# Kernel optimization log

Measured on AMD Instinct MI355X. Metric: run time of the kernel, lower is better.

Reference implementation:

```python
import jax, jax.numpy as jnp
import numpy as np

K = 3
PAD = (K - 1) // 2


def _conv1d(x, w, b):
    # x: [B, T, C]; w: [F, C, K] (torch OIH layout); conv over T, 'same' padding
    y = jax.lax.conv_general_dilated(x.transpose(0, 2, 1), w, (1,), [(PAD, PAD)],
                                     dimension_numbers=('NCH', 'OIH', 'NCH'))
    return (y + b[None, :, None]).transpose(0, 2, 1)


def _ln(x, g, b, eps=1e-5):
    m = x.mean(-1, keepdims=True)
    v = ((x - m) ** 2).mean(-1, keepdims=True)
    return (x - m) * jax.lax.rsqrt(v + eps) * g + b


def _predictor(x, p):
    # Conv1d -> ReLU -> LN -> Conv1d -> ReLU -> LN -> Linear(F,1) -> ReLU -> squeeze
    w1, b1, g1, be1, w2, b2, g2, be2, wl, bl = p
    h = _ln(jax.nn.relu(_conv1d(x, w1, b1)), g1, be1)
    h = _ln(jax.nn.relu(_conv1d(h, w2, b2)), g2, be2)
    return jax.nn.relu(jnp.einsum('btf,f->bt', h, wl) + bl)  # [B, T]


def _length_regulate(x, dur, max_len):
    # Gather-based frame expansion: frame t comes from token i = searchsorted(cumsum(dur), t, 'right')
    cs = jnp.cumsum(dur, axis=1)                       # [B, T]
    t = jnp.arange(max_len)                            # [M]
    idx = jax.vmap(lambda c: jnp.searchsorted(c, t, side='right'))(cs)  # [B, M]
    valid = t[None, :] < cs[:, -1:]                    # [B, M]
    idx = jnp.minimum(idx, x.shape[1] - 1)
    out = jnp.take_along_axis(x, idx[:, :, None], axis=1)  # [B, M, C]
    out = jnp.where(valid[:, :, None], out, jnp.zeros((), x.dtype))
    mel_len = jnp.minimum(cs[:, -1], max_len)
    return out, mel_len


def _bucketize(x, boundaries):
    # torch.bucketize(right=False): first boundary > x  ==  searchsorted(side='right')
    return jnp.searchsorted(boundaries, x, side='right')


def setup_inputs() -> dict:
    key = jax.random.key(0)
    ks = jax.random.split(key, 12)
    B, T, M, C, F, NB = 32, 256, 2048, 256, 256, 256
    inp = {}
    inp['inputs'] = jax.random.normal(ks[0], (B, T, C), jnp.float32)
    inp['true_duration'] = jax.random.randint(ks[1], (B, T), 0, 16)
    inp['true_pitch'] = jax.random.uniform(ks[2], (B, M), jnp.float32) * 300.0
    inp['true_energy'] = jax.random.uniform(ks[3], (B, M), jnp.float32) * 200.0
    inp['mel_max_len'] = M
    inp['pitch_q'] = jnp.linspace(0.0, 300.0, NB - 1)
    inp['energy_q'] = jnp.linspace(0.0, 200.0, NB - 1)

    def pred_params(k, cin):
        kk = jax.random.split(k, 3)
        return [0.02 * jax.random.normal(kk[0], (F, cin, K)), jnp.zeros((F,)),
                jnp.ones((F,)), jnp.zeros((F,)),
                0.02 * jax.random.normal(kk[1], (F, F, K)), jnp.zeros((F,)),
                jnp.ones((F,)), jnp.zeros((F,)),
                0.02 * jax.random.normal(kk[2], (F,)), jnp.zeros(())]

    names = ['w1', 'b1', 'g1', 'be1', 'w2', 'b2', 'g2', 'be2', 'wl', 'bl']
    for i, pre in enumerate(['dp', 'pp', 'ep']):
        for n, v in zip(names, pred_params(ks[4 + i], C)):
            inp[pre + '_' + n] = v
    inp['pitch_emb'] = 0.02 * jax.random.normal(ks[8], (NB, C))
    inp['energy_emb'] = 0.02 * jax.random.normal(ks[9], (NB, C))
    return inp


def reference(inputs, true_duration, true_pitch, true_energy, mel_max_len,
              pitch_q, energy_q,
              dp_w1, dp_b1, dp_g1, dp_be1, dp_w2, dp_b2, dp_g2, dp_be2, dp_wl, dp_bl,
              pp_w1, pp_b1, pp_g1, pp_be1, pp_w2, pp_b2, pp_g2, pp_be2, pp_wl, pp_bl,
              ep_w1, ep_b1, ep_g1, ep_be1, ep_w2, ep_b2, ep_g2, ep_be2, ep_wl, ep_bl,
              pitch_emb, energy_emb):
    # Training path: expansion uses true_duration, embeddings use true pitch/energy.
    dp = (dp_w1, dp_b1, dp_g1, dp_be1, dp_w2, dp_b2, dp_g2, dp_be2, dp_wl, dp_bl)
    pp = (pp_w1, pp_b1, pp_g1, pp_be1, pp_w2, pp_b2, pp_g2, pp_be2, pp_wl, pp_bl)
    ep = (ep_w1, ep_b1, ep_g1, ep_be1, ep_w2, ep_b2, ep_g2, ep_be2, ep_wl, ep_bl)
    durations = _predictor(inputs, dp)                       # [B, T], alpha=1.0
    outputs, mel_len = _length_regulate(inputs, true_duration, mel_max_len)  # [B, M, C]
    pitches = _predictor(outputs, pp)                        # [B, M]
    outputs = outputs + pitch_emb[_bucketize(true_pitch, pitch_q)]
    energies = _predictor(outputs, ep)                       # [B, M]
    outputs = outputs + energy_emb[_bucketize(true_energy, energy_q)]
    return outputs, durations, pitches, energies, mel_len
```

## Files before the change

kernel.cpp:

```cpp
#include <hip/hip_runtime.h>
#include <hip/hip_bf16.h>
#include <stdint.h>

#define DUR_OFF 16777216
#define PIT_OFF 16785408
#define ENE_OFF 16850944
#define MEL_OFF 16916480

typedef __attribute__((ext_vector_type(8))) short short8;
typedef __attribute__((ext_vector_type(4))) float f32x4;

__device__ __forceinline__ void async16(const void* g, void* l) {
  __builtin_amdgcn_global_load_lds((__attribute__((address_space(1))) void*)g,
                                   (__attribute__((address_space(3))) void*)l, 16, 0, 0);
}

__device__ __forceinline__ unsigned short bfu(float f) {
  __hip_bfloat16 h = __float2bfloat16(f);
  return __builtin_bit_cast(unsigned short, h);
}
__device__ __forceinline__ float f_from_bf(unsigned short u) {
  return __builtin_bit_cast(float, (unsigned)u << 16);
}

__global__ void zero2_kernel(__hip_bfloat16* __restrict__ xb, __hip_bfloat16* __restrict__ h1,
                             __hip_bfloat16* __restrict__ M1, __hip_bfloat16* __restrict__ M2) {
  int buf = blockIdx.x >> 6, sub = blockIdx.x & 63;
  int b = sub >> 1, top = sub & 1;
  __hip_bfloat16* p; int L;
  if (buf == 0) { p = xb; L = 256; }
  else if (buf == 1) { p = h1; L = 256; }
  else if (buf == 2) { p = M1; L = 2048; }
  else { p = M2; L = 2048; }
  size_t row = (size_t)b * (L + 2) + (top ? (L + 1) : 0);
  p[row * 256 + threadIdx.x] = __float2bfloat16(0.0f);
}

__global__ void packfrag_kernel(const float* __restrict__ w0, const float* __restrict__ w1,
                                const float* __restrict__ w2, const float* __restrict__ w3,
                                const float* __restrict__ w4, const float* __restrict__ w5,
                                __hip_bfloat16* __restrict__ wpbase) {
  int t = blockIdx.x * 256 + threadIdx.x;
  int wsel = t / 24576;
  int rem = t % 24576;
  const float* w = wsel == 0 ? w0 : wsel == 1 ? w1 : wsel == 2 ? w2
                 : wsel == 3 ? w3 : wsel == 4 ? w4 : w5;
  __hip_bfloat16* wp = wpbase + (size_t)wsel * 196608;
  int L = rem & 63;
  int ks = (rem >> 6) & 7;
  int q = rem >> 9;
  int tap = q % 3, r = q / 3;
  int ni = r & 3, fb = r >> 2;
  int f = fb * 64 + ni * 16 + (L & 15);
  int cb = ks * 32 + ((L >> 4) << 3);
  short8 o;
#pragma unroll
  for (int e = 0; e < 8; ++e)
    o[e] = (short)bfu(w[((size_t)f * 256 + cb + e) * 3 + tap]);
  *(short8*)(wp + (size_t)rem * 8) = o;
}

__global__ void cvt_pad_kernel(const float* __restrict__ x, __hip_bfloat16* __restrict__ xb) {
  int idx = blockIdx.x * 256 + threadIdx.x;
  float4 v = ((const float4*)x)[idx];
  int c4 = idx & 63;
  int rowi = idx >> 6;
  int b = rowi >> 8, t = rowi & 255;
  ushort4 o;
  o.x = bfu(v.x); o.y = bfu(v.y); o.z = bfu(v.z); o.w = bfu(v.w);
  ((ushort4*)(xb + ((size_t)b * 258 + t + 1) * 256))[c4] = o;
}

__global__ void gather_kernel(const float* __restrict__ x, const int* __restrict__ dur,
                              __hip_bfloat16* __restrict__ outB, float* __restrict__ mel) {
  __shared__ int scs[256];
  __shared__ int sidx[64];
  __shared__ int sval[64];
  int bch = blockIdx.x >> 5;
  int m0 = (blockIdx.x & 31) << 6;
  int tid = threadIdx.x;
  scs[tid] = dur[bch * 256 + tid];
  __syncthreads();
  for (int off = 1; off < 256; off <<= 1) {
    int add = (tid >= off) ? scs[tid - off] : 0;
    __syncthreads();
    scs[tid] += add;
    __syncthreads();
  }
  int total = scs[255];
  if (tid == 0 && (blockIdx.x & 31) == 0)
    mel[bch] = (float)(total < 2048 ? total : 2048);
  if (tid < 64) {
    int m = m0 + tid;
    int lo = 0, hi = 256;
    while (lo < hi) { int mid = (lo + hi) >> 1; if (scs[mid] <= m) lo = mid + 1; else hi = mid; }
    sidx[tid] = lo < 255 ? lo : 255;
    sval[tid] = (m < total);
  }
  __syncthreads();
  int lane = tid & 63, rs = tid >> 6;
  for (int r = rs; r < 64; r += 4) {
    float4 v = make_float4(0.f, 0.f, 0.f, 0.f);
    if (sval[r]) v = ((const float4*)(x + ((size_t)bch * 256 + sidx[r]) * 256))[lane];
    ushort4 o;
    o.x = bfu(v.x); o.y = bfu(v.y); o.z = bfu(v.z); o.w = bfu(v.w);
    ((ushort4*)(outB + ((size_t)bch * 2050 + m0 + r + 1) * 256))[lane] = o;
  }
}

__global__ void addemb_kernel(const float* __restrict__ tp, const float* __restrict__ te,
                              const float* __restrict__ pq, const float* __restrict__ eq,
                              const float* __restrict__ pemb, const float* __restrict__ eemb,
                              const __hip_bfloat16* __restrict__ M1, __hip_bfloat16* __restrict__ M2,
                              float* __restrict__ out) {
  __shared__ float sp[255], se[255];
  __shared__ int sip[64], sie[64];
  int bch = blockIdx.x >> 5;
  int m0 = (blockIdx.x & 31) << 6;
  int tid = threadIdx.x;
  if (tid < 255) { sp[tid] = pq[tid]; se[tid] = eq[tid]; }
  __syncthreads();
  if (tid < 64) {
    float xv = tp[bch * 2048 + m0 + tid];
    int lo = 0, hi = 255;
    while (lo < hi) { int mid = (lo + hi) >> 1; if (sp[mid] <= xv) lo = mid + 1; else hi = mid; }
    sip[tid] = lo;
    float ev = te[bch * 2048 + m0 + tid];
    lo = 0; hi = 255;
    while (lo < hi) { int mid = (lo + hi) >> 1; if (se[mid] <= ev) lo = mid + 1; else hi = mid; }
    sie[tid] = lo;
  }
  __syncthreads();
  int lane = tid & 63, rs = tid >> 6;
  for (int r = rs; r < 64; r += 4) {
    ushort4 mv = ((const ushort4*)(M1 + ((size_t)bch * 2050 + m0 + r + 1) * 256))[lane];
    float4 ep = ((const float4*)(pemb + (size_t)sip[r] * 256))[lane];
    float4 ee = ((const float4*)(eemb + (size_t)sie[r] * 256))[lane];
    float4 v;
    v.x = f_from_bf(mv.x) + ep.x; v.y = f_from_bf(mv.y) + ep.y;
    v.z = f_from_bf(mv.z) + ep.z; v.w = f_from_bf(mv.w) + ep.w;
    ushort4 o;
    o.x = bfu(v.x); o.y = bfu(v.y); o.z = bfu(v.z); o.w = bfu(v.w);
    ((ushort4*)(M2 + ((size_t)bch * 2050 + m0 + r + 1) * 256))[lane] = o;
    float4 w;
    w.x = v.x + ee.x; w.y = v.y + ee.y; w.z = v.z + ee.z; w.w = v.w + ee.w;
    ((float4*)(out + ((size_t)bch * 2048 + m0 + r) * 256))[lane] = w;
  }
}

__device__ __forceinline__ void loadB4(const char* Wb, int s, short8* dst) {
  int tap = s >> 3, ks = s & 7;
#pragma unroll
  for (int ni = 0; ni < 4; ++ni)
    dst[ni] = *(const short8*)(Wb + ((((ni * 3 + tap) << 3) + ks) << 10));
}

template <int EPI, int TM>
__global__ __launch_bounds__(256, 2)
void pred_gemm(const __hip_bfloat16* __restrict__ Ap, const __hip_bfloat16* __restrict__ Wf,
               const float* __restrict__ bias, const float* __restrict__ gamma,
               const float* __restrict__ beta, const float* __restrict__ wl,
               const float* __restrict__ blp, __hip_bfloat16* __restrict__ Hout,
               float* __restrict__ Sout, int L) {
  constexpr int MI = TM / 16;
  constexpr int ABYTES = (TM + 2) * 512;
  __shared__ char lA[ABYTES];
  __shared__ float lred[TM * 8];
  __shared__ float lstat[TM * 2];

  const int tid = threadIdx.x;
  const int wid = tid >> 6;
  const int lane = tid & 63;
  const int wn = wid;
  const int tiles = L / TM;
  const int b = blockIdx.x / tiles;
  const int t0 = (blockIdx.x % tiles) * TM;

  const char* Asrc = (const char*)(Ap + ((size_t)b * (L + 2) + t0) * 256);
#pragma unroll
  for (int j = 0; j < (ABYTES + 4095) / 4096; ++j) {
    int off = j * 4096 + tid * 16;
    if (off < ABYTES) {
      int so = off ^ (((off >> 9) & 7) << 4);
      async16(Asrc + so, lA + off);
    }
  }

  const char* Wb = (const char*)Wf + (size_t)wn * 98304 + lane * 16;

  f32x4 acc[MI][4];
  const f32x4 zero4 = {0.f, 0.f, 0.f, 0.f};
#pragma unroll
  for (int i = 0; i < MI; ++i)
#pragma unroll
    for (int j = 0; j < 4; ++j) acc[i][j] = zero4;

  short8 bA[4], bB[4];
  loadB4(Wb, 0, bA);

  __syncthreads();

  const int rlane = lane & 15;
  const int colp = (lane >> 4) << 4;
#pragma unroll
  for (int s = 0; s < 24; ++s) {
    const int tap = s >> 3, ks = s & 7;
    short8* cur = (s & 1) ? bB : bA;
    short8* nxt = (s & 1) ? bA : bB;
    if (s < 23) loadB4(Wb, s + 1, nxt);
    const int xorv = ((tap + rlane) & 7) << 4;
    short8 av[MI];
#pragma unroll
    for (int mi = 0; mi < MI; ++mi) {
      int a = (tap + (mi << 4) + rlane) * 512 + (ks << 6) + colp;
      av[mi] = *(const short8*)(lA + (a ^ xorv));
    }
#pragma unroll
    for (int mi = 0; mi < MI; ++mi)
#pragma unroll
      for (int ni = 0; ni < 4; ++ni)
        acc[mi][ni] =
            __builtin_amdgcn_mfma_f32_16x16x32_bf16(av[mi], cur[ni], acc[mi][ni], 0, 0, 0);
  }

  const int cb0 = (wn << 6) + rlane;
  float bi[4], gg[4], bb[4];
#pragma unroll
  for (int ni = 0; ni < 4; ++ni) {
    int col = cb0 + (ni << 4);
    bi[ni] = bias[col]; gg[ni] = gamma[col]; bb[ni] = beta[col];
  }
  const int rbase = (lane >> 4) << 2;
#pragma unroll
  for (int mi = 0; mi < MI; ++mi) {
#pragma unroll
    for (int j = 0; j < 4; ++j) {
      float s = 0.f, s2 = 0.f;
#pragma unroll
      for (int ni = 0; ni < 4; ++ni) {
        float r = fmaxf(acc[mi][ni][j] + bi[ni], 0.f);
        s += r; s2 += r * r;
      }
#pragma unroll
      for (int d = 1; d < 16; d <<= 1) { s += __shfl_xor(s, d); s2 += __shfl_xor(s2, d); }
      if ((lane & 15) == 0) {
        int row = (mi << 4) + rbase + j;
        lred[row * 8 + wn] = s;
        lred[row * 8 + 4 + wn] = s2;
      }
    }
  }
  __syncthreads();
  if (tid < TM) {
    float s = lred[tid * 8] + lred[tid * 8 + 1] + lred[tid * 8 + 2] + lred[tid * 8 + 3];
    float s2 = lred[tid * 8 + 4] + lred[tid * 8 + 5] + lred[tid * 8 + 6] + lred[tid * 8 + 7];
    float mean = s * (1.f / 256.f);
    float var = fmaxf(s2 * (1.f / 256.f) - mean * mean, 0.f);
    lstat[tid * 2] = mean;
    lstat[tid * 2 + 1] = rsqrtf(var + 1e-5f);
  }
  __syncthreads();

  if constexpr (EPI == 0) {
#pragma unroll
    for (int mi = 0; mi < MI; ++mi) {
#pragma unroll
      for (int j = 0; j < 4; ++j) {
        int row = (mi << 4) + rbase + j;
        float mean = lstat[row * 2], rstd = lstat[row * 2 + 1];
        __hip_bfloat16* hp = Hout + ((size_t)b * (L + 2) + t0 + row + 1) * 256 + cb0;
#pragma unroll
        for (int ni = 0; ni < 4; ++ni) {
          float r = fmaxf(acc[mi][ni][j] + bi[ni], 0.f);
          hp[ni << 4] = __float2bfloat16((r - mean) * rstd * gg[ni] + bb[ni]);
        }
      }
    }
  } else {
    float wlv[4];
#pragma unroll
    for (int ni = 0; ni < 4; ++ni) wlv[ni] = wl[cb0 + (ni << 4)];
#pragma unroll
    for (int mi = 0; mi < MI; ++mi) {
#pragma unroll
      for (int j = 0; j < 4; ++j) {
        int row = (mi << 4) + rbase + j;
        float mean = lstat[row * 2], rstd = lstat[row * 2 + 1];
        float ds = 0.f;
#pragma unroll
        for (int ni = 0; ni < 4; ++ni) {
          float r = fmaxf(acc[mi][ni][j] + bi[ni], 0.f);
          ds += ((r - mean) * rstd * gg[ni] + bb[ni]) * wlv[ni];
        }
#pragma unroll
        for (int d = 1; d < 16; d <<= 1) ds += __shfl_xor(ds, d);
        if ((lane & 15) == 0) lred[row * 8 + wn] = ds;
      }
    }
    __syncthreads();
    if (tid < TM) {
      float z = lred[tid * 8] + lred[tid * 8 + 1] + lred[tid * 8 + 2] + lred[tid * 8 + 3] + blp[0];
      Sout[(size_t)b * L + t0 + tid] = fmaxf(z, 0.f);
    }
  }
}

extern "C" void kernel_launch(void* const* d_in, const int* in_sizes, int n_in,
                              void* d_out, int out_size, void* d_ws, size_t ws_size,
                              hipStream_t stream) {
  const float* x = (const float*)d_in[0];
  const int* dur = (const int*)d_in[1];
  const float* tp = (const float*)d_in[2];
  const float* te = (const float*)d_in[3];
  const float* pq = (const float*)d_in[5];
  const float* eq = (const float*)d_in[6];
  const float* pemb = (const float*)d_in[37];
  const float* eemb = (const float*)d_in[38];

  char* ws = (char*)d_ws;
  __hip_bfloat16* wpb = (__hip_bfloat16*)ws;
  __hip_bfloat16* wp[6];
  for (int i = 0; i < 6; ++i) wp[i] = wpb + (size_t)i * 196608;
  __hip_bfloat16* xb = (__hip_bfloat16*)(ws + 2359296);
  __hip_bfloat16* h1dp = (__hip_bfloat16*)(ws + 6586368);
  __hip_bfloat16* M1 = (__hip_bfloat16*)(ws + 10813440);
  __hip_bfloat16* M2 = (__hip_bfloat16*)(ws + 44400640);

  float* out = (float*)d_out;

  zero2_kernel<<<256, 256, 0, stream>>>(xb, h1dp, M1, M2);
  packfrag_kernel<<<576, 256, 0, stream>>>((const float*)d_in[7], (const float*)d_in[11],
                                           (const float*)d_in[17], (const float*)d_in[21],
                                           (const float*)d_in[27], (const float*)d_in[31], wpb);
  cvt_pad_kernel<<<2048, 256, 0, stream>>>(x, xb);

  pred_gemm<0, 64><<<128, 256, 0, stream>>>(xb, wp[0], (const float*)d_in[8],
                                            (const float*)d_in[9], (const float*)d_in[10],
                                            nullptr, nullptr, h1dp, nullptr, 256);
  pred_gemm<1, 64><<<128, 256, 0, stream>>>(h1dp, wp[1], (const float*)d_in[12],
                                            (const float*)d_in[13], (const float*)d_in[14],
                                            (const float*)d_in[15], (const float*)d_in[16],
                                            nullptr, out + DUR_OFF, 256);

  gather_kernel<<<1024, 256, 0, stream>>>(x, dur, M1, out + MEL_OFF);

  pred_gemm<0, 128><<<512, 256, 0, stream>>>(M1, wp[2], (const float*)d_in[18],
                                             (const float*)d_in[19], (const float*)d_in[20],
                                             nullptr, nullptr, M2, nullptr, 2048);
  pred_gemm<1, 128><<<512, 256, 0, stream>>>(M2, wp[3], (const float*)d_in[22],
                                             (const float*)d_in[23], (const float*)d_in[24],
                                             (const float*)d_in[25], (const float*)d_in[26],
                                             nullptr, out + PIT_OFF, 2048);

  addemb_kernel<<<1024, 256, 0, stream>>>(tp, te, pq, eq, pemb, eemb, M1, M2, out);

  pred_gemm<0, 128><<<512, 256, 0, stream>>>(M2, wp[4], (const float*)d_in[28],
                                             (const float*)d_in[29], (const float*)d_in[30],
                                             nullptr, nullptr, M1, nullptr, 2048);
  pred_gemm<1, 128><<<512, 256, 0, stream>>>(M1, wp[5], (const float*)d_in[32],
                                             (const float*)d_in[33], (const float*)d_in[34],
                                             (const float*)d_in[35], (const float*)d_in[36],
                                             nullptr, out + ENE_OFF, 2048);
}
```

Baseline: 375.2 us.

## Halve GEMM row tiles, raise occupancy, roll k-loop, gather from bf16 copy

The predictor GEMM row tile is halved (128 to 64 for the mel-length predictors, 64 to 32 for the duration predictor), which doubles the grid. Launch bounds rise to three blocks per SM, and the fully unrolled 24-slice MFMA loop becomes a rolled loop of 12 iterations, each handling two slices with ping-pong B-fragment prefetch. Together these aim to cut register pressure and improve occupancy and wave count, at the cost of reloading the weight fragments for twice as many tiles. The gather kernel now reads the already-converted bf16 padded input instead of fp32, halving its read traffic and skipping the conversion.

```diff
diff --git a/kernel.cpp b/kernel.cpp
--- a/kernel.cpp
+++ b/kernel.cpp
@@ -71,7 +71,7 @@
   ((ushort4*)(xb + ((size_t)b * 258 + t + 1) * 256))[c4] = o;
 }
 
-__global__ void gather_kernel(const float* __restrict__ x, const int* __restrict__ dur,
+__global__ void gather_kernel(const __hip_bfloat16* __restrict__ xb, const int* __restrict__ dur,
                               __hip_bfloat16* __restrict__ outB, float* __restrict__ mel) {
   __shared__ int scs[256];
   __shared__ int sidx[64];
@@ -100,10 +100,9 @@
   __syncthreads();
   int lane = tid & 63, rs = tid >> 6;
   for (int r = rs; r < 64; r += 4) {
-    float4 v = make_float4(0.f, 0.f, 0.f, 0.f);
-    if (sval[r]) v = ((const float4*)(x + ((size_t)bch * 256 + sidx[r]) * 256))[lane];
-    ushort4 o;
-    o.x = bfu(v.x); o.y = bfu(v.y); o.z = bfu(v.z); o.w = bfu(v.w);
+    ushort4 o = make_ushort4(0, 0, 0, 0);
+    if (sval[r])
+      o = ((const ushort4*)(xb + ((size_t)bch * 258 + sidx[r] + 1) * 256))[lane];
     ((ushort4*)(outB + ((size_t)bch * 2050 + m0 + r + 1) * 256))[lane] = o;
   }
 }
@@ -148,15 +147,33 @@
   }
 }
 
-__device__ __forceinline__ void loadB4(const char* Wb, int s, short8* dst) {
+__device__ __forceinline__ void loadB4(const char* Wb, int s, short8 (&dst)[4]) {
   int tap = s >> 3, ks = s & 7;
 #pragma unroll
   for (int ni = 0; ni < 4; ++ni)
     dst[ni] = *(const short8*)(Wb + ((((ni * 3 + tap) << 3) + ks) << 10));
 }
 
+template <int MI>
+__device__ __forceinline__ void sliceMFMA(int s, const char* lA, int rlane, int colp,
+                                          const short8 (&bv)[4], f32x4 (&acc)[MI][4]) {
+  const int tap = s >> 3, ks = s & 7;
+  const int xorv = ((tap + rlane) & 7) << 4;
+  short8 av[MI];
+#pragma unroll
+  for (int mi = 0; mi < MI; ++mi) {
+    int a = (tap + (mi << 4) + rlane) * 512 + (ks << 6) + colp;
+    av[mi] = *(const short8*)(lA + (a ^ xorv));
+  }
+#pragma unroll
+  for (int mi = 0; mi < MI; ++mi)
+#pragma unroll
+    for (int ni = 0; ni < 4; ++ni)
+      acc[mi][ni] = __builtin_amdgcn_mfma_f32_16x16x32_bf16(av[mi], bv[ni], acc[mi][ni], 0, 0, 0);
+}
+
 template <int EPI, int TM>
-__global__ __launch_bounds__(256, 2)
+__global__ __launch_bounds__(256, 3)
 void pred_gemm(const __hip_bfloat16* __restrict__ Ap, const __hip_bfloat16* __restrict__ Wf,
                const float* __restrict__ bias, const float* __restrict__ gamma,
                const float* __restrict__ beta, const float* __restrict__ wl,
@@ -195,32 +212,19 @@
 #pragma unroll
     for (int j = 0; j < 4; ++j) acc[i][j] = zero4;
 
-  short8 bA[4], bB[4];
-  loadB4(Wb, 0, bA);
+  short8 pA[4], pB[4];
+  loadB4(Wb, 0, pA);
 
   __syncthreads();
 
   const int rlane = lane & 15;
   const int colp = (lane >> 4) << 4;
-#pragma unroll
-  for (int s = 0; s < 24; ++s) {
-    const int tap = s >> 3, ks = s & 7;
-    short8* cur = (s & 1) ? bB : bA;
-    short8* nxt = (s & 1) ? bA : bB;
-    if (s < 23) loadB4(Wb, s + 1, nxt);
-    const int xorv = ((tap + rlane) & 7) << 4;
-    short8 av[MI];
-#pragma unroll
-    for (int mi = 0; mi < MI; ++mi) {
-      int a = (tap + (mi << 4) + rlane) * 512 + (ks << 6) + colp;
-      av[mi] = *(const short8*)(lA + (a ^ xorv));
-    }
-#pragma unroll
-    for (int mi = 0; mi < MI; ++mi)
-#pragma unroll
-      for (int ni = 0; ni < 4; ++ni)
-        acc[mi][ni] =
-            __builtin_amdgcn_mfma_f32_16x16x32_bf16(av[mi], cur[ni], acc[mi][ni], 0, 0, 0);
+#pragma unroll 1
+  for (int s2 = 0; s2 < 12; ++s2) {
+    loadB4(Wb, 2 * s2 + 1, pB);
+    sliceMFMA<MI>(2 * s2, lA, rlane, colp, pA, acc);
+    if (s2 < 11) loadB4(Wb, 2 * s2 + 2, pA);
+    sliceMFMA<MI>(2 * s2 + 1, lA, rlane, colp, pB, acc);
   }
 
   const int cb0 = (wn << 6) + rlane;
@@ -334,30 +338,30 @@
                                            (const float*)d_in[27], (const float*)d_in[31], wpb);
   cvt_pad_kernel<<<2048, 256, 0, stream>>>(x, xb);
 
-  pred_gemm<0, 64><<<128, 256, 0, stream>>>(xb, wp[0], (const float*)d_in[8],
+  pred_gemm<0, 32><<<256, 256, 0, stream>>>(xb, wp[0], (const float*)d_in[8],
                                             (const float*)d_in[9], (const float*)d_in[10],
                                             nullptr, nullptr, h1dp, nullptr, 256);
-  pred_gemm<1, 64><<<128, 256, 0, stream>>>(h1dp, wp[1], (const float*)d_in[12],
+  pred_gemm<1, 32><<<256, 256, 0, stream>>>(h1dp, wp[1], (const float*)d_in[12],
                                             (const float*)d_in[13], (const float*)d_in[14],
                                             (const float*)d_in[15], (const float*)d_in[16],
                                             nullptr, out + DUR_OFF, 256);
 
-  gather_kernel<<<1024, 256, 0, stream>>>(x, dur, M1, out + MEL_OFF);
-
-  pred_gemm<0, 128><<<512, 256, 0, stream>>>(M1, wp[2], (const float*)d_in[18],
+  gather_kernel<<<1024, 256, 0, stream>>>(xb, dur, M1, out + MEL_OFF);
+
+  pred_gemm<0, 64><<<1024, 256, 0, stream>>>(M1, wp[2], (const float*)d_in[18],
                                              (const float*)d_in[19], (const float*)d_in[20],
                                              nullptr, nullptr, M2, nullptr, 2048);
-  pred_gemm<1, 128><<<512, 256, 0, stream>>>(M2, wp[3], (const float*)d_in[22],
+  pred_gemm<1, 64><<<1024, 256, 0, stream>>>(M2, wp[3], (const float*)d_in[22],
                                              (const float*)d_in[23], (const float*)d_in[24],
                                              (const float*)d_in[25], (const float*)d_in[26],
                                              nullptr, out + PIT_OFF, 2048);
 
   addemb_kernel<<<1024, 256, 0, stream>>>(tp, te, pq, eq, pemb, eemb, M1, M2, out);
 
-  pred_gemm<0, 128><<<512, 256, 0, stream>>>(M2, wp[4], (const float*)d_in[28],
+  pred_gemm<0, 64><<<1024, 256, 0, stream>>>(M2, wp[4], (const float*)d_in[28],
                                              (const float*)d_in[29], (const float*)d_in[30],
                                              nullptr, nullptr, M1, nullptr, 2048);
-  pred_gemm<1, 128><<<512, 256, 0, stream>>>(M1, wp[5], (const float*)d_in[32],
+  pred_gemm<1, 64><<<1024, 256, 0, stream>>>(M1, wp[5], (const float*)d_in[32],
                                              (const float*)d_in[33], (const float*)d_in[34],
                                              (const float*)d_in[35], (const float*)d_in[36],
                                              nullptr, out + ENE_OFF, 2048);
```

New measurement: 348.2 us. 1.08x faster.
